# Performance work log

Hardware: AMD Instinct MI355X
Metric: run time of the kernel (lower is better)

Reference implementation:

```python
import jax, jax.numpy as jnp
import numpy as np

EPS = 1e-8
ACT_BITS = 8


def _ternary_vq(t):
    gamma = jnp.abs(t).mean()
    q = jnp.clip(jnp.round(t / (gamma + EPS)), -1.0, 1.0)
    return q * gamma


def setup_inputs() -> dict:
    key = jax.random.key(0)
    k1, k2, k3 = jax.random.split(key, 3)
    in_features, out_features = 1024, 1024
    x = jax.random.normal(k1, (8, 4096, in_features), dtype=jnp.float32)
    weight = jax.random.normal(k2, (out_features, in_features), dtype=jnp.float32)
    bias = jax.random.normal(k3, (out_features,), dtype=jnp.float32)
    return {"x": x, "weight": weight, "bias": bias}


def reference(x, weight, bias):
    # Weight/bias ternary quantization (done once in __init__ of the module)
    wq = _ternary_vq(weight)   # [out, in]
    bq = _ternary_vq(bias)     # [out]

    # Activation quantization: power-of-two scale from global absmax
    qmax = jnp.float32(2 ** (ACT_BITS - 1) - 1)  # 127
    max_val = jnp.max(jnp.abs(x))
    scale = jnp.exp2(jnp.floor(jnp.log2(max_val / qmax + EPS)))
    xq = jnp.round(jnp.clip(x, -qmax * scale, qmax * scale) / scale) * scale

    # F.linear: x @ W^T + b
    return jnp.einsum('bsi,oi->bso', xq, wq) + bq
```

## Files before the change

kernel.cpp:

```cpp
#include <hip/hip_runtime.h>

typedef __attribute__((ext_vector_type(4))) int int4v;

constexpr int Mdim = 32768;
constexpr int Kdim = 1024;
constexpr int Ndim = 1024;
constexpr float FEPS = 1e-8f;

constexpr size_t WQ_OFF = 32768;
constexpr size_t XQ_OFF = WQ_OFF + (size_t)Ndim * Kdim;
constexpr size_t WS_NEED = XQ_OFF + (size_t)Mdim * Kdim;

__global__ void k_absmax(const uint4* __restrict__ xv, unsigned* __restrict__ pmax, int n4) {
  int i0 = blockIdx.x * blockDim.x + threadIdx.x;
  int stride = gridDim.x * blockDim.x;
  unsigned m = 0u;
  for (int i = i0; i < n4; i += stride) {
    uint4 v = xv[i];
    m = max(m, v.x & 0x7fffffffu);
    m = max(m, v.y & 0x7fffffffu);
    m = max(m, v.z & 0x7fffffffu);
    m = max(m, v.w & 0x7fffffffu);
  }
  #pragma unroll
  for (int off = 32; off > 0; off >>= 1)
    m = max(m, (unsigned)__shfl_down((int)m, off, 64));
  __shared__ unsigned red[4];
  if ((threadIdx.x & 63) == 0) red[threadIdx.x >> 6] = m;
  __syncthreads();
  if (threadIdx.x == 0) {
    unsigned r = max(max(red[0], red[1]), max(red[2], red[3]));
    pmax[blockIdx.x] = r;
  }
}

__global__ void k_wsum(const float4* __restrict__ wv, float* __restrict__ partials, int n4) {
  float s = 0.f;
  int stride = gridDim.x * blockDim.x;
  for (int i = blockIdx.x * blockDim.x + threadIdx.x; i < n4; i += stride) {
    float4 v = wv[i];
    s += fabsf(v.x) + fabsf(v.y) + fabsf(v.z) + fabsf(v.w);
  }
  __shared__ float red[256];
  red[threadIdx.x] = s;
  __syncthreads();
  for (int h = 128; h > 0; h >>= 1) {
    if (threadIdx.x < h) red[threadIdx.x] += red[threadIdx.x + h];
    __syncthreads();
  }
  if (threadIdx.x == 0) partials[blockIdx.x] = red[0];
}

__global__ void k_finalize(const float* __restrict__ bias, const float* __restrict__ partials,
                           const unsigned* __restrict__ pmax,
                           float* __restrict__ scalars, float* __restrict__ bq) {
  __shared__ float redf[256];
  __shared__ unsigned redu[256];
  __shared__ float sh_gb;
  int t = threadIdx.x;

  float s = fabsf(bias[t]) + fabsf(bias[t + 256]) + fabsf(bias[t + 512]) + fabsf(bias[t + 768]);
  redf[t] = s;
  unsigned m = 0u;
  #pragma unroll
  for (int i = 0; i < 8; ++i) m = max(m, pmax[t + 256 * i]);
  redu[t] = m;
  __syncthreads();
  for (int h = 128; h > 0; h >>= 1) {
    if (t < h) {
      redf[t] += redf[t + h];
      redu[t] = max(redu[t], redu[t + h]);
    }
    __syncthreads();
  }
  if (t == 0) {
    float gb = redf[0] / 1024.0f;
    float sw = 0.f;
    for (int i = 0; i < 256; ++i) sw += partials[i];
    float gw = sw / (1024.0f * 1024.0f);
    float maxval = __uint_as_float(redu[0]);
    float v = maxval / 127.0f + FEPS;
    int e = (int)((__float_as_uint(v) >> 23) & 0xff) - 127;
    float scale = ldexpf(1.0f, e);
    scalars[0] = gw;
    scalars[1] = gb;
    scalars[2] = scale;
    scalars[3] = scale * gw;
    scalars[4] = 127.0f * scale;
    scalars[5] = ldexpf(1.0f, -e);
    sh_gb = gb;
  }
  __syncthreads();
  float gb = sh_gb;
  for (int i = t; i < 1024; i += 256) {
    float q = rintf(bias[i] / (gb + FEPS));
    q = fminf(fmaxf(q, -1.0f), 1.0f);
    bq[i] = q * gb;
  }
}

__device__ __forceinline__ int qact8(float v, float qs, float inv) {
  return (int)rintf(fminf(fmaxf(v, -qs), qs) * inv);
}

__global__ void k_wquant(const float* __restrict__ w, const float* __restrict__ scalars,
                         unsigned char* __restrict__ wq) {
  float inv_g = scalars[0] + FEPS;
  int wave = (blockIdx.x * blockDim.x + threadIdx.x) >> 6;
  int lane = threadIdx.x & 63;
  int nb = wave >> 4;
  int kt = wave & 15;
  int r = lane >> 2;
  int c = lane & 3;
  const float4* src = (const float4*)(w + (size_t)(nb * 16 + r) * Kdim + kt * 64 + c * 16);
  unsigned o[4];
  #pragma unroll
  for (int v = 0; v < 4; ++v) {
    float4 f = src[v];
    int a = (int)rintf(fminf(fmaxf(f.x / inv_g, -1.f), 1.f));
    int b = (int)rintf(fminf(fmaxf(f.y / inv_g, -1.f), 1.f));
    int cc = (int)rintf(fminf(fmaxf(f.z / inv_g, -1.f), 1.f));
    int d = (int)rintf(fminf(fmaxf(f.w / inv_g, -1.f), 1.f));
    o[v] = (unsigned)(a & 0xff) | ((unsigned)(b & 0xff) << 8) |
           ((unsigned)(cc & 0xff) << 16) | ((unsigned)(d & 0xff) << 24);
  }
  uint4 pk; pk.x = o[0]; pk.y = o[1]; pk.z = o[2]; pk.w = o[3];
  *(uint4*)(wq + (size_t)wave * 1024 + c * 256 + r * 16) = pk;
}

__global__ void k_xquant(const float* __restrict__ x, const float* __restrict__ scalars,
                         unsigned char* __restrict__ xq) {
  float qs = scalars[4], inv = scalars[5];
  int wave = (blockIdx.x * blockDim.x + threadIdx.x) >> 6;
  int lane = threadIdx.x & 63;
  int mb = wave >> 4;
  int kt = wave & 15;
  int r = lane >> 2;
  int c = lane & 3;
  const float4* src = (const float4*)(x + (size_t)(mb * 16 + r) * Kdim + kt * 64 + c * 16);
  unsigned o[4];
  #pragma unroll
  for (int v = 0; v < 4; ++v) {
    float4 f = src[v];
    o[v] = (unsigned)(qact8(f.x, qs, inv) & 0xff) |
           ((unsigned)(qact8(f.y, qs, inv) & 0xff) << 8) |
           ((unsigned)(qact8(f.z, qs, inv) & 0xff) << 16) |
           ((unsigned)(qact8(f.w, qs, inv) & 0xff) << 24);
  }
  uint4 pk; pk.x = o[0]; pk.y = o[1]; pk.z = o[2]; pk.w = o[3];
  *(uint4*)(xq + (size_t)wave * 1024 + c * 256 + r * 16) = pk;
}

__launch_bounds__(256)
__global__ void k_gemm(const unsigned char* __restrict__ xq, const unsigned char* __restrict__ wq,
                       const float* __restrict__ scalars, const float* __restrict__ bq,
                       float* __restrict__ out) {
  const int tid = threadIdx.x;
  const int lane = tid & 63;
  const int wv = tid >> 6;
  const int wr = wv >> 1;
  const int wc = wv & 1;

  int bid = blockIdx.x;
  int swz = (bid & 7) * ((int)gridDim.x >> 3) + (bid >> 3);
  const int mtile = swz >> 3;
  const int ntile = swz & 7;
  const int m0 = mtile * 128;
  const int n0 = ntile * 128;

  const unsigned char* Abase = xq + ((size_t)(m0 / 16 + wr * 4) * 16) * 1024 + lane * 16;
  const unsigned char* Bbase = wq + ((size_t)(n0 / 16 + wc * 4) * 16) * 1024 + lane * 16;

  int4v acc[4][4];
  #pragma unroll
  for (int i = 0; i < 4; ++i)
    #pragma unroll
    for (int j = 0; j < 4; ++j)
      acc[i][j] = (int4v){0, 0, 0, 0};

  int4v a0[4], b0[4], a1[4], b1[4];

#define LOADF(abuf, bbuf, kt) do {                                            \
    _Pragma("unroll")                                                         \
    for (int mi = 0; mi < 4; ++mi)                                            \
      abuf[mi] = *(const int4v*)(Abase + ((size_t)mi * 16 + (kt)) * 1024);    \
    _Pragma("unroll")                                                         \
    for (int ni = 0; ni < 4; ++ni)                                            \
      bbuf[ni] = *(const int4v*)(Bbase + ((size_t)ni * 16 + (kt)) * 1024);    \
  } while (0)

#define MFMAS(abuf, bbuf) do {                                                \
    _Pragma("unroll")                                                         \
    for (int mi = 0; mi < 4; ++mi)                                            \
      _Pragma("unroll")                                                       \
      for (int ni = 0; ni < 4; ++ni)                                          \
        acc[mi][ni] = __builtin_amdgcn_mfma_i32_16x16x64_i8(abuf[mi], bbuf[ni], acc[mi][ni], 0, 0, 0); \
  } while (0)

  LOADF(a0, b0, 0);
  #pragma unroll
  for (int kt = 0; kt < 16; kt += 2) {
    if (kt + 1 < 16) LOADF(a1, b1, kt + 1);
    MFMAS(a0, b0);
    if (kt + 2 < 16) LOADF(a0, b0, kt + 2);
    MFMAS(a1, b1);
  }
#undef LOADF
#undef MFMAS

  const float sg = scalars[3];
  const int fr = lane & 15;
  #pragma unroll
  for (int ni = 0; ni < 4; ++ni) {
    const int col = n0 + wc * 64 + ni * 16 + fr;
    const float bb = bq[col];
    #pragma unroll
    for (int mi = 0; mi < 4; ++mi) {
      const int rowb = m0 + wr * 64 + mi * 16 + (lane >> 4) * 4;
      #pragma unroll
      for (int r = 0; r < 4; ++r)
        out[(size_t)(rowb + r) * Ndim + col] = (float)acc[mi][ni][r] * sg + bb;
    }
  }
}

extern "C" void kernel_launch(void* const* d_in, const int* in_sizes, int n_in,
                              void* d_out, int out_size, void* d_ws, size_t ws_size,
                              hipStream_t stream) {
  const float* x = (const float*)d_in[0];
  const float* weight = (const float*)d_in[1];
  const float* bias = (const float*)d_in[2];
  float* out = (float*)d_out;

  if (ws_size < WS_NEED) return;

  char* ws = (char*)d_ws;
  float* scalars = (float*)ws;
  float* partials = (float*)(ws + 1024);
  unsigned* pmax = (unsigned*)(ws + 4096);
  float* bq = (float*)(ws + 16384);
  unsigned char* wq = (unsigned char*)(ws + WQ_OFF);
  unsigned char* xq = (unsigned char*)(ws + XQ_OFF);

  k_absmax<<<2048, 256, 0, stream>>>((const uint4*)x, pmax, Mdim * Kdim / 4);
  k_wsum<<<256, 256, 0, stream>>>((const float4*)weight, partials, Ndim * Kdim / 4);
  k_finalize<<<1, 256, 0, stream>>>(bias, partials, pmax, scalars, bq);
  k_wquant<<<256, 256, 0, stream>>>(weight, scalars, wq);
  k_xquant<<<8192, 256, 0, stream>>>(x, scalars, xq);
  k_gemm<<<2048, 256, 0, stream>>>(xq, wq, scalars, bq, out);
}
```

Baseline: 118.6 us.

## Stage GEMM tiles through LDS with async global_load_lds triple buffering

The int8 GEMM now loads its A and B tiles through direct global-to-LDS copies into a three-stage ring buffer. Previously each wave read its operands straight from global memory into registers, so the two waves that share a row or column tile fetched the same data twice. Loads now run two k-steps ahead of the MFMAs, with vmcnt waits and a barrier once per step. The cost is 48KB of LDS per block, which may limit occupancy, plus barrier synchronisation overhead.

```diff
diff --git a/kernel.cpp b/kernel.cpp
--- a/kernel.cpp
+++ b/kernel.cpp
@@ -10,6 +10,12 @@
 constexpr size_t WQ_OFF = 32768;
 constexpr size_t XQ_OFF = WQ_OFF + (size_t)Ndim * Kdim;
 constexpr size_t WS_NEED = XQ_OFF + (size_t)Mdim * Kdim;
+
+__device__ __forceinline__ void gload16(const void* g, void* l) {
+  __builtin_amdgcn_global_load_lds(
+      (const __attribute__((address_space(1))) unsigned int*)g,
+      (__attribute__((address_space(3))) unsigned int*)l, 16, 0, 0);
+}
 
 __global__ void k_absmax(const uint4* __restrict__ xv, unsigned* __restrict__ pmax, int n4) {
   int i0 = blockIdx.x * blockDim.x + threadIdx.x;
@@ -155,6 +161,8 @@
 __global__ void k_gemm(const unsigned char* __restrict__ xq, const unsigned char* __restrict__ wq,
                        const float* __restrict__ scalars, const float* __restrict__ bq,
                        float* __restrict__ out) {
+  __shared__ __align__(16) unsigned char lds[3 * 16384];
+
   const int tid = threadIdx.x;
   const int lane = tid & 63;
   const int wv = tid >> 6;
@@ -168,8 +176,20 @@
   const int m0 = mtile * 128;
   const int n0 = ntile * 128;
 
-  const unsigned char* Abase = xq + ((size_t)(m0 / 16 + wr * 4) * 16) * 1024 + lane * 16;
-  const unsigned char* Bbase = wq + ((size_t)(n0 / 16 + wc * 4) * 16) * 1024 + lane * 16;
+  const unsigned char* gA0 = xq + ((size_t)(mtile * 8 + wv) * 16) * 1024 + lane * 16;
+  const unsigned char* gA1 = xq + ((size_t)(mtile * 8 + wv + 4) * 16) * 1024 + lane * 16;
+  const unsigned char* gB0 = wq + ((size_t)(ntile * 8 + wv) * 16) * 1024 + lane * 16;
+  const unsigned char* gB1 = wq + ((size_t)(ntile * 8 + wv + 4) * 16) * 1024 + lane * 16;
+  const int lA0 = wv * 1024, lA1 = (wv + 4) * 1024;
+  const int lB0 = 8192 + wv * 1024, lB1 = 8192 + (wv + 4) * 1024;
+
+#define STAGE(kt, buf) do {                                   \
+    unsigned char* base_ = lds + (buf) * 16384;               \
+    gload16(gA0 + (size_t)(kt) * 1024, base_ + lA0);          \
+    gload16(gA1 + (size_t)(kt) * 1024, base_ + lA1);          \
+    gload16(gB0 + (size_t)(kt) * 1024, base_ + lB0);          \
+    gload16(gB1 + (size_t)(kt) * 1024, base_ + lB1);          \
+  } while (0)
 
   int4v acc[4][4];
   #pragma unroll
@@ -178,35 +198,55 @@
     for (int j = 0; j < 4; ++j)
       acc[i][j] = (int4v){0, 0, 0, 0};
 
-  int4v a0[4], b0[4], a1[4], b1[4];
-
-#define LOADF(abuf, bbuf, kt) do {                                            \
-    _Pragma("unroll")                                                         \
-    for (int mi = 0; mi < 4; ++mi)                                            \
-      abuf[mi] = *(const int4v*)(Abase + ((size_t)mi * 16 + (kt)) * 1024);    \
-    _Pragma("unroll")                                                         \
-    for (int ni = 0; ni < 4; ++ni)                                            \
-      bbuf[ni] = *(const int4v*)(Bbase + ((size_t)ni * 16 + (kt)) * 1024);    \
-  } while (0)
-
-#define MFMAS(abuf, bbuf) do {                                                \
-    _Pragma("unroll")                                                         \
-    for (int mi = 0; mi < 4; ++mi)                                            \
-      _Pragma("unroll")                                                       \
-      for (int ni = 0; ni < 4; ++ni)                                          \
-        acc[mi][ni] = __builtin_amdgcn_mfma_i32_16x16x64_i8(abuf[mi], bbuf[ni], acc[mi][ni], 0, 0, 0); \
-  } while (0)
-
-  LOADF(a0, b0, 0);
-  #pragma unroll
-  for (int kt = 0; kt < 16; kt += 2) {
-    if (kt + 1 < 16) LOADF(a1, b1, kt + 1);
-    MFMAS(a0, b0);
-    if (kt + 2 < 16) LOADF(a0, b0, kt + 2);
-    MFMAS(a1, b1);
-  }
-#undef LOADF
-#undef MFMAS
+  const int aoff = wr * 4 * 1024 + lane * 16;
+  const int boff = 8192 + wc * 4 * 1024 + lane * 16;
+
+  STAGE(0, 0);
+  STAGE(1, 1);
+
+  int cur = 0;
+  for (int kt = 0; kt < 15; ++kt) {
+    asm volatile("s_waitcnt vmcnt(4)" ::: "memory");
+    __builtin_amdgcn_s_barrier();
+    asm volatile("" ::: "memory");
+    const unsigned char* bufp = lds + cur * 16384;
+    int4v a[4], b[4];
+    #pragma unroll
+    for (int mi = 0; mi < 4; ++mi)
+      a[mi] = *(const int4v*)(bufp + aoff + mi * 1024);
+    #pragma unroll
+    for (int ni = 0; ni < 4; ++ni)
+      b[ni] = *(const int4v*)(bufp + boff + ni * 1024);
+    if (kt < 14) {
+      int nb = cur + 2; if (nb >= 3) nb -= 3;
+      STAGE(kt + 2, nb);
+    }
+    #pragma unroll
+    for (int mi = 0; mi < 4; ++mi)
+      #pragma unroll
+      for (int ni = 0; ni < 4; ++ni)
+        acc[mi][ni] = __builtin_amdgcn_mfma_i32_16x16x64_i8(a[mi], b[ni], acc[mi][ni], 0, 0, 0);
+    cur = (cur == 2) ? 0 : cur + 1;
+  }
+  asm volatile("s_waitcnt vmcnt(0)" ::: "memory");
+  __builtin_amdgcn_s_barrier();
+  asm volatile("" ::: "memory");
+  {
+    const unsigned char* bufp = lds + cur * 16384;
+    int4v a[4], b[4];
+    #pragma unroll
+    for (int mi = 0; mi < 4; ++mi)
+      a[mi] = *(const int4v*)(bufp + aoff + mi * 1024);
+    #pragma unroll
+    for (int ni = 0; ni < 4; ++ni)
+      b[ni] = *(const int4v*)(bufp + boff + ni * 1024);
+    #pragma unroll
+    for (int mi = 0; mi < 4; ++mi)
+      #pragma unroll
+      for (int ni = 0; ni < 4; ++ni)
+        acc[mi][ni] = __builtin_amdgcn_mfma_i32_16x16x64_i8(a[mi], b[ni], acc[mi][ni], 0, 0, 0);
+  }
+#undef STAGE
 
   const float sg = scalars[3];
   const int fr = lane & 15;
```

New measurement: 112.2 us. -5.4%, faster.

## Fuse activation quantization into GEMM via LDS and merge preprocessing kernels

Applied to the files above, without the earlier changes.

Merges the absmax and weight-sum reductions into one launch, and folds weight quantization into the finalize kernel so each block reduces the weight partials itself. The separate int8 activation buffer is removed: a new 1024-thread GEMM kernel quantizes a 128-row stripe of x directly into 128 KB of LDS, then sweeps all 1024 output columns in four passes. This is meant to cut the xq global write and read-back plus two launches. In exchange it gives one block per CU with a serial quantize-then-compute phase, less register blocking per wave, and weight tiles reloaded from global for every k-step without double buffering.

```diff
diff --git a/kernel.cpp b/kernel.cpp
--- a/kernel.cpp
+++ b/kernel.cpp
@@ -8,76 +8,111 @@
 constexpr float FEPS = 1e-8f;
 
 constexpr size_t WQ_OFF = 32768;
-constexpr size_t XQ_OFF = WQ_OFF + (size_t)Ndim * Kdim;
-constexpr size_t WS_NEED = XQ_OFF + (size_t)Mdim * Kdim;
-
-__global__ void k_absmax(const uint4* __restrict__ xv, unsigned* __restrict__ pmax, int n4) {
-  int i0 = blockIdx.x * blockDim.x + threadIdx.x;
-  int stride = gridDim.x * blockDim.x;
-  unsigned m = 0u;
-  for (int i = i0; i < n4; i += stride) {
-    uint4 v = xv[i];
-    m = max(m, v.x & 0x7fffffffu);
-    m = max(m, v.y & 0x7fffffffu);
-    m = max(m, v.z & 0x7fffffffu);
-    m = max(m, v.w & 0x7fffffffu);
-  }
-  #pragma unroll
-  for (int off = 32; off > 0; off >>= 1)
-    m = max(m, (unsigned)__shfl_down((int)m, off, 64));
-  __shared__ unsigned red[4];
-  if ((threadIdx.x & 63) == 0) red[threadIdx.x >> 6] = m;
-  __syncthreads();
-  if (threadIdx.x == 0) {
-    unsigned r = max(max(red[0], red[1]), max(red[2], red[3]));
-    pmax[blockIdx.x] = r;
-  }
-}
-
-__global__ void k_wsum(const float4* __restrict__ wv, float* __restrict__ partials, int n4) {
-  float s = 0.f;
-  int stride = gridDim.x * blockDim.x;
-  for (int i = blockIdx.x * blockDim.x + threadIdx.x; i < n4; i += stride) {
-    float4 v = wv[i];
-    s += fabsf(v.x) + fabsf(v.y) + fabsf(v.z) + fabsf(v.w);
-  }
+constexpr size_t WS_NEED = WQ_OFF + (size_t)Ndim * Kdim;
+
+__global__ void k_pre(const uint4* __restrict__ xv, const float4* __restrict__ wv,
+                      unsigned* __restrict__ pmax, float* __restrict__ partials) {
+  const int tid = threadIdx.x;
+  if (blockIdx.x < 2048) {
+    int i0 = blockIdx.x * 256 + tid;
+    const int stride = 2048 * 256;
+    const int n4 = Mdim * Kdim / 4;
+    unsigned m = 0u;
+    for (int i = i0; i < n4; i += stride) {
+      uint4 v = xv[i];
+      m = max(m, v.x & 0x7fffffffu);
+      m = max(m, v.y & 0x7fffffffu);
+      m = max(m, v.z & 0x7fffffffu);
+      m = max(m, v.w & 0x7fffffffu);
+    }
+    #pragma unroll
+    for (int off = 32; off > 0; off >>= 1)
+      m = max(m, (unsigned)__shfl_down((int)m, off, 64));
+    __shared__ unsigned red[4];
+    if ((tid & 63) == 0) red[tid >> 6] = m;
+    __syncthreads();
+    if (tid == 0)
+      pmax[blockIdx.x] = max(max(red[0], red[1]), max(red[2], red[3]));
+  } else {
+    int wb = blockIdx.x - 2048;
+    float s = 0.f;
+    const int stride = 256 * 256;
+    const int n4 = Ndim * Kdim / 4;
+    for (int i = wb * 256 + tid; i < n4; i += stride) {
+      float4 v = wv[i];
+      s += fabsf(v.x) + fabsf(v.y) + fabsf(v.z) + fabsf(v.w);
+    }
+    __shared__ float red[256];
+    red[tid] = s;
+    __syncthreads();
+    for (int h = 128; h > 0; h >>= 1) {
+      if (tid < h) red[tid] += red[tid + h];
+      __syncthreads();
+    }
+    if (tid == 0) partials[wb] = red[0];
+  }
+}
+
+__global__ void k_finalize2(const float* __restrict__ bias, const float* __restrict__ w,
+                            const float* __restrict__ partials, const unsigned* __restrict__ pmax,
+                            float* __restrict__ scalars, float* __restrict__ bq,
+                            unsigned char* __restrict__ wq) {
   __shared__ float red[256];
-  red[threadIdx.x] = s;
+  const int t = threadIdx.x;
+  const int b = blockIdx.x;
+
+  red[t] = partials[t];
   __syncthreads();
   for (int h = 128; h > 0; h >>= 1) {
-    if (threadIdx.x < h) red[threadIdx.x] += red[threadIdx.x + h];
-    __syncthreads();
-  }
-  if (threadIdx.x == 0) partials[blockIdx.x] = red[0];
-}
-
-__global__ void k_finalize(const float* __restrict__ bias, const float* __restrict__ partials,
-                           const unsigned* __restrict__ pmax,
-                           float* __restrict__ scalars, float* __restrict__ bq) {
-  __shared__ float redf[256];
+    if (t < h) red[t] += red[t + h];
+    __syncthreads();
+  }
+  const float gw = red[0] / (1024.0f * 1024.0f);
+  __syncthreads();
+  const float inv_g = gw + FEPS;
+
+  {
+    const int tile = b * 4 + (t >> 6);
+    const int nb = tile >> 4;
+    const int kt = tile & 15;
+    const int l = t & 63;
+    const float4* src = (const float4*)(w + (size_t)(nb * 16 + (l >> 2)) * Kdim + kt * 64 + (l & 3) * 16);
+    unsigned o[4];
+    #pragma unroll
+    for (int v = 0; v < 4; ++v) {
+      float4 f = src[v];
+      int a  = (int)rintf(fminf(fmaxf(f.x / inv_g, -1.f), 1.f));
+      int bb = (int)rintf(fminf(fmaxf(f.y / inv_g, -1.f), 1.f));
+      int cc = (int)rintf(fminf(fmaxf(f.z / inv_g, -1.f), 1.f));
+      int dd = (int)rintf(fminf(fmaxf(f.w / inv_g, -1.f), 1.f));
+      o[v] = (unsigned)(a & 0xff) | ((unsigned)(bb & 0xff) << 8) |
+             ((unsigned)(cc & 0xff) << 16) | ((unsigned)(dd & 0xff) << 24);
+    }
+    uint4 pk; pk.x = o[0]; pk.y = o[1]; pk.z = o[2]; pk.w = o[3];
+    const int lp = (l >> 2) | ((l & 3) << 4);
+    *(uint4*)(wq + (size_t)tile * 1024 + lp * 16) = pk;
+  }
+
+  if (b != 0) return;
+
   __shared__ unsigned redu[256];
   __shared__ float sh_gb;
-  int t = threadIdx.x;
-
-  float s = fabsf(bias[t]) + fabsf(bias[t + 256]) + fabsf(bias[t + 512]) + fabsf(bias[t + 768]);
-  redf[t] = s;
   unsigned m = 0u;
   #pragma unroll
   for (int i = 0; i < 8; ++i) m = max(m, pmax[t + 256 * i]);
   redu[t] = m;
+  float s = fabsf(bias[t]) + fabsf(bias[t + 256]) + fabsf(bias[t + 512]) + fabsf(bias[t + 768]);
+  red[t] = s;
   __syncthreads();
   for (int h = 128; h > 0; h >>= 1) {
     if (t < h) {
-      redf[t] += redf[t + h];
+      red[t] += red[t + h];
       redu[t] = max(redu[t], redu[t + h]);
     }
     __syncthreads();
   }
   if (t == 0) {
-    float gb = redf[0] / 1024.0f;
-    float sw = 0.f;
-    for (int i = 0; i < 256; ++i) sw += partials[i];
-    float gw = sw / (1024.0f * 1024.0f);
+    float gb = red[0] / 1024.0f;
     float maxval = __uint_as_float(redu[0]);
     float v = maxval / 127.0f + FEPS;
     int e = (int)((__float_as_uint(v) >> 23) & 0xff) - 127;
@@ -99,127 +134,87 @@
   }
 }
 
-__device__ __forceinline__ int qact8(float v, float qs, float inv) {
-  return (int)rintf(fminf(fmaxf(v, -qs), qs) * inv);
-}
-
-__global__ void k_wquant(const float* __restrict__ w, const float* __restrict__ scalars,
-                         unsigned char* __restrict__ wq) {
-  float inv_g = scalars[0] + FEPS;
-  int wave = (blockIdx.x * blockDim.x + threadIdx.x) >> 6;
-  int lane = threadIdx.x & 63;
-  int nb = wave >> 4;
-  int kt = wave & 15;
-  int r = lane >> 2;
-  int c = lane & 3;
-  const float4* src = (const float4*)(w + (size_t)(nb * 16 + r) * Kdim + kt * 64 + c * 16);
-  unsigned o[4];
-  #pragma unroll
-  for (int v = 0; v < 4; ++v) {
-    float4 f = src[v];
-    int a = (int)rintf(fminf(fmaxf(f.x / inv_g, -1.f), 1.f));
-    int b = (int)rintf(fminf(fmaxf(f.y / inv_g, -1.f), 1.f));
-    int cc = (int)rintf(fminf(fmaxf(f.z / inv_g, -1.f), 1.f));
-    int d = (int)rintf(fminf(fmaxf(f.w / inv_g, -1.f), 1.f));
-    o[v] = (unsigned)(a & 0xff) | ((unsigned)(b & 0xff) << 8) |
-           ((unsigned)(cc & 0xff) << 16) | ((unsigned)(d & 0xff) << 24);
-  }
-  uint4 pk; pk.x = o[0]; pk.y = o[1]; pk.z = o[2]; pk.w = o[3];
-  *(uint4*)(wq + (size_t)wave * 1024 + c * 256 + r * 16) = pk;
-}
-
-__global__ void k_xquant(const float* __restrict__ x, const float* __restrict__ scalars,
-                         unsigned char* __restrict__ xq) {
-  float qs = scalars[4], inv = scalars[5];
-  int wave = (blockIdx.x * blockDim.x + threadIdx.x) >> 6;
-  int lane = threadIdx.x & 63;
-  int mb = wave >> 4;
-  int kt = wave & 15;
-  int r = lane >> 2;
-  int c = lane & 3;
-  const float4* src = (const float4*)(x + (size_t)(mb * 16 + r) * Kdim + kt * 64 + c * 16);
-  unsigned o[4];
-  #pragma unroll
-  for (int v = 0; v < 4; ++v) {
-    float4 f = src[v];
-    o[v] = (unsigned)(qact8(f.x, qs, inv) & 0xff) |
-           ((unsigned)(qact8(f.y, qs, inv) & 0xff) << 8) |
-           ((unsigned)(qact8(f.z, qs, inv) & 0xff) << 16) |
-           ((unsigned)(qact8(f.w, qs, inv) & 0xff) << 24);
-  }
-  uint4 pk; pk.x = o[0]; pk.y = o[1]; pk.z = o[2]; pk.w = o[3];
-  *(uint4*)(xq + (size_t)wave * 1024 + c * 256 + r * 16) = pk;
-}
-
-__launch_bounds__(256)
-__global__ void k_gemm(const unsigned char* __restrict__ xq, const unsigned char* __restrict__ wq,
-                       const float* __restrict__ scalars, const float* __restrict__ bq,
-                       float* __restrict__ out) {
+__launch_bounds__(1024)
+__global__ void k_megagemm(const float* __restrict__ x, const unsigned char* __restrict__ wq,
+                           const float* __restrict__ scalars, const float* __restrict__ bq,
+                           float* __restrict__ out) {
+  __shared__ __align__(16) unsigned char Alds[131072];
+
   const int tid = threadIdx.x;
   const int lane = tid & 63;
   const int wv = tid >> 6;
-  const int wr = wv >> 1;
-  const int wc = wv & 1;
-
-  int bid = blockIdx.x;
-  int swz = (bid & 7) * ((int)gridDim.x >> 3) + (bid >> 3);
-  const int mtile = swz >> 3;
-  const int ntile = swz & 7;
-  const int m0 = mtile * 128;
-  const int n0 = ntile * 128;
-
-  const unsigned char* Abase = xq + ((size_t)(m0 / 16 + wr * 4) * 16) * 1024 + lane * 16;
-  const unsigned char* Bbase = wq + ((size_t)(n0 / 16 + wc * 4) * 16) * 1024 + lane * 16;
-
-  int4v acc[4][4];
+  const int mtile = blockIdx.x;
+  const float qs = scalars[4], inv = scalars[5];
+
   #pragma unroll
-  for (int i = 0; i < 4; ++i)
-    #pragma unroll
-    for (int j = 0; j < 4; ++j)
-      acc[i][j] = (int4v){0, 0, 0, 0};
-
-  int4v a0[4], b0[4], a1[4], b1[4];
-
-#define LOADF(abuf, bbuf, kt) do {                                            \
-    _Pragma("unroll")                                                         \
-    for (int mi = 0; mi < 4; ++mi)                                            \
-      abuf[mi] = *(const int4v*)(Abase + ((size_t)mi * 16 + (kt)) * 1024);    \
-    _Pragma("unroll")                                                         \
-    for (int ni = 0; ni < 4; ++ni)                                            \
-      bbuf[ni] = *(const int4v*)(Bbase + ((size_t)ni * 16 + (kt)) * 1024);    \
-  } while (0)
-
-#define MFMAS(abuf, bbuf) do {                                                \
-    _Pragma("unroll")                                                         \
-    for (int mi = 0; mi < 4; ++mi)                                            \
-      _Pragma("unroll")                                                       \
-      for (int ni = 0; ni < 4; ++ni)                                          \
-        acc[mi][ni] = __builtin_amdgcn_mfma_i32_16x16x64_i8(abuf[mi], bbuf[ni], acc[mi][ni], 0, 0, 0); \
-  } while (0)
-
-  LOADF(a0, b0, 0);
-  #pragma unroll
-  for (int kt = 0; kt < 16; kt += 2) {
-    if (kt + 1 < 16) LOADF(a1, b1, kt + 1);
-    MFMAS(a0, b0);
-    if (kt + 2 < 16) LOADF(a0, b0, kt + 2);
-    MFMAS(a1, b1);
-  }
-#undef LOADF
-#undef MFMAS
-
+  for (int i = 0; i < 8; ++i) {
+    const int tile = wv * 8 + i;
+    const int mb = tile >> 4;
+    const int kt = tile & 15;
+    const float4* src = (const float4*)(x + (size_t)(mtile * 128 + mb * 16 + (lane >> 2)) * Kdim
+                                          + kt * 64 + (lane & 3) * 16);
+    unsigned o[4];
+    #pragma unroll
+    for (int v = 0; v < 4; ++v) {
+      float4 f = src[v];
+      int a = (int)rintf(fminf(fmaxf(f.x, -qs), qs) * inv);
+      int b = (int)rintf(fminf(fmaxf(f.y, -qs), qs) * inv);
+      int c = (int)rintf(fminf(fmaxf(f.z, -qs), qs) * inv);
+      int d = (int)rintf(fminf(fmaxf(f.w, -qs), qs) * inv);
+      o[v] = (unsigned)(a & 0xff) | ((unsigned)(b & 0xff) << 8) |
+             ((unsigned)(c & 0xff) << 16) | ((unsigned)(d & 0xff) << 24);
+    }
+    uint4 pk; pk.x = o[0]; pk.y = o[1]; pk.z = o[2]; pk.w = o[3];
+    const int lp = (lane >> 2) | ((lane & 3) << 4);
+    *(uint4*)(Alds + (size_t)tile * 1024 + lp * 16) = pk;
+  }
+  __syncthreads();
+
+  const int wr = wv >> 2;
+  const int wc = wv & 3;
   const float sg = scalars[3];
-  const int fr = lane & 15;
-  #pragma unroll
-  for (int ni = 0; ni < 4; ++ni) {
-    const int col = n0 + wc * 64 + ni * 16 + fr;
-    const float bb = bq[col];
-    #pragma unroll
-    for (int mi = 0; mi < 4; ++mi) {
-      const int rowb = m0 + wr * 64 + mi * 16 + (lane >> 4) * 4;
+  const unsigned char* Alds_a0 = Alds + (size_t)(wr * 2) * 16 * 1024 + lane * 16;
+  const unsigned char* Alds_a1 = Alds + (size_t)(wr * 2 + 1) * 16 * 1024 + lane * 16;
+
+  for (int np = 0; np < 4; ++np) {
+    int4v acc[2][4];
+    #pragma unroll
+    for (int i = 0; i < 2; ++i)
       #pragma unroll
-      for (int r = 0; r < 4; ++r)
-        out[(size_t)(rowb + r) * Ndim + col] = (float)acc[mi][ni][r] * sg + bb;
+      for (int j = 0; j < 4; ++j)
+        acc[i][j] = (int4v){0, 0, 0, 0};
+
+    const unsigned char* Bb = wq + ((size_t)(np * 16 + wc * 4) * 16) * 1024 + lane * 16;
+
+    #pragma unroll
+    for (int kt = 0; kt < 16; ++kt) {
+      int4v b0 = *(const int4v*)(Bb + (size_t)(0 * 16 + kt) * 1024);
+      int4v b1 = *(const int4v*)(Bb + (size_t)(1 * 16 + kt) * 1024);
+      int4v b2 = *(const int4v*)(Bb + (size_t)(2 * 16 + kt) * 1024);
+      int4v b3 = *(const int4v*)(Bb + (size_t)(3 * 16 + kt) * 1024);
+      int4v a0 = *(const int4v*)(Alds_a0 + (size_t)kt * 1024);
+      int4v a1 = *(const int4v*)(Alds_a1 + (size_t)kt * 1024);
+      acc[0][0] = __builtin_amdgcn_mfma_i32_16x16x64_i8(a0, b0, acc[0][0], 0, 0, 0);
+      acc[0][1] = __builtin_amdgcn_mfma_i32_16x16x64_i8(a0, b1, acc[0][1], 0, 0, 0);
+      acc[0][2] = __builtin_amdgcn_mfma_i32_16x16x64_i8(a0, b2, acc[0][2], 0, 0, 0);
+      acc[0][3] = __builtin_amdgcn_mfma_i32_16x16x64_i8(a0, b3, acc[0][3], 0, 0, 0);
+      acc[1][0] = __builtin_amdgcn_mfma_i32_16x16x64_i8(a1, b0, acc[1][0], 0, 0, 0);
+      acc[1][1] = __builtin_amdgcn_mfma_i32_16x16x64_i8(a1, b1, acc[1][1], 0, 0, 0);
+      acc[1][2] = __builtin_amdgcn_mfma_i32_16x16x64_i8(a1, b2, acc[1][2], 0, 0, 0);
+      acc[1][3] = __builtin_amdgcn_mfma_i32_16x16x64_i8(a1, b3, acc[1][3], 0, 0, 0);
+    }
+
+    #pragma unroll
+    for (int ni = 0; ni < 4; ++ni) {
+      const int col = np * 256 + wc * 64 + ni * 16 + (lane & 15);
+      const float bb = bq[col];
+      #pragma unroll
+      for (int mi = 0; mi < 2; ++mi) {
+        const int rowb = mtile * 128 + wr * 32 + mi * 16 + (lane >> 4) * 4;
+        #pragma unroll
+        for (int r = 0; r < 4; ++r)
+          out[(size_t)(rowb + r) * Ndim + col] = (float)acc[mi][ni][r] * sg + bb;
+      }
     }
   }
 }
@@ -240,12 +235,8 @@
   unsigned* pmax = (unsigned*)(ws + 4096);
   float* bq = (float*)(ws + 16384);
   unsigned char* wq = (unsigned char*)(ws + WQ_OFF);
-  unsigned char* xq = (unsigned char*)(ws + XQ_OFF);
-
-  k_absmax<<<2048, 256, 0, stream>>>((const uint4*)x, pmax, Mdim * Kdim / 4);
-  k_wsum<<<256, 256, 0, stream>>>((const float4*)weight, partials, Ndim * Kdim / 4);
-  k_finalize<<<1, 256, 0, stream>>>(bias, partials, pmax, scalars, bq);
-  k_wquant<<<256, 256, 0, stream>>>(weight, scalars, wq);
-  k_xquant<<<8192, 256, 0, stream>>>(x, scalars, xq);
-  k_gemm<<<2048, 256, 0, stream>>>(xq, wq, scalars, bq, out);
-}
+
+  k_pre<<<2304, 256, 0, stream>>>((const uint4*)x, (const float4*)weight, pmax, partials);
+  k_finalize2<<<256, 256, 0, stream>>>(bias, weight, partials, pmax, scalars, bq, wq);
+  k_megagemm<<<256, 1024, 0, stream>>>(x, wq, scalars, bq, out);
+}
```

After: 95.94 us. 19.1% less time.
